# Kernel optimization log

Measured on AMD Instinct MI355X. Metric: run time of the kernel, lower is better.

The kernel has to match this reference:

```python
import jax, jax.numpy as jnp
import numpy as np

L, D_IN, D_MODEL, N_LAYERS = 4096, 8, 256, 2
ED, N, K = 512, 16, 4          # d_inner = 2*d_model, d_state, d_conv
DT_RANK = 16                   # ceil(d_model/16)
EPS = 1e-5


def setup_inputs() -> dict:
    key = jax.random.key(0)
    ks = jax.random.split(key, 10)
    def g(k, shape, s=0.02):
        return jax.random.normal(k, shape, jnp.float32) * s
    A_init = jnp.tile(jnp.arange(1, N + 1, dtype=jnp.float32), (N_LAYERS, ED, 1))
    return {
        "x": jax.random.normal(ks[0], (L, D_IN), jnp.float32),
        "fc_in_w": g(ks[1], (D_MODEL, D_IN), 0.1),
        "fc_in_b": jnp.zeros((D_MODEL,), jnp.float32),
        "fc_out_w": g(ks[2], (1, D_MODEL), 0.1),
        "fc_out_b": jnp.zeros((1,), jnp.float32),
        "norm_w": jnp.ones((N_LAYERS, D_MODEL), jnp.float32),
        "in_proj_w": g(ks[3], (N_LAYERS, 2 * ED, D_MODEL)),
        "conv_w": g(ks[4], (N_LAYERS, ED, 1, K), 0.1),
        "conv_b": jnp.zeros((N_LAYERS, ED), jnp.float32),
        "x_proj_w": g(ks[5], (N_LAYERS, DT_RANK + 2 * N, ED)),
        "dt_proj_w": g(ks[6], (N_LAYERS, ED, DT_RANK), 0.1),
        "dt_proj_b": jnp.full((N_LAYERS, ED), -4.0, jnp.float32),  # softplus(-4)~0.018
        "A_log": jnp.log(A_init),
        "D": jnp.ones((N_LAYERS, ED), jnp.float32),
        "out_proj_w": g(ks[7], (N_LAYERS, D_MODEL, ED)),
    }


def rmsnorm(x, w):
    return x * jax.lax.rsqrt(jnp.mean(x * x, axis=-1, keepdims=True) + EPS) * w


def causal_depthwise_conv(x, w, b):
    # x: [L, ED], w: [ED, 1, K] -> causal depthwise conv along L
    y = jax.lax.conv_general_dilated(
        x.T[None],  # [1, ED, L]
        w, (1,), [(K - 1, 0)],
        dimension_numbers=("NCH", "OIH", "NCH"),
        feature_group_count=ED)
    return y[0].T + b  # [L, ED]


def mamba_block(x, p):
    norm_w, in_w, cw, cb, xp_w, dtw, dtb, a_log, d, out_w = p
    xn = rmsnorm(x, norm_w)
    xz = xn @ in_w.T                      # [L, 2*ED]
    xi, z = xz[:, :ED], xz[:, ED:]
    xc = jax.nn.silu(causal_depthwise_conv(xi, cw, cb))   # [L, ED]
    dbc = xc @ xp_w.T                     # [L, DT_RANK + 2N]
    delta = jax.nn.softplus(dbc[:, :DT_RANK] @ dtw.T + dtb)  # [L, ED]
    B = dbc[:, DT_RANK:DT_RANK + N]       # [L, N]
    C = dbc[:, DT_RANK + N:]              # [L, N]
    A = -jnp.exp(a_log)                   # [ED, N]
    dA = jnp.exp(delta[:, :, None] * A[None])                 # [L, ED, N]
    dBx = delta[:, :, None] * B[:, None, :] * xc[:, :, None]  # [L, ED, N]

    def step(h, inp):
        da, dbx, c = inp
        h = da * h + dbx                  # [ED, N]
        return h, jnp.einsum("en,n->e", h, c)

    _, ys = jax.lax.scan(step, jnp.zeros((ED, N), x.dtype), (dA, dBx, C))
    y = (ys + d * xc) * jax.nn.silu(z)
    return x + y @ out_w.T


def forward(x, fc_in_w, fc_in_b, fc_out_w, fc_out_b, norm_w, in_proj_w, conv_w,
            conv_b, x_proj_w, dt_proj_w, dt_proj_b, A_log, D, out_proj_w):
    h = x @ fc_in_w.T + fc_in_b           # [L, D_MODEL]

    def layer(h, p):
        return mamba_block(h, p), None

    h, _ = jax.lax.scan(layer, h, (norm_w, in_proj_w, conv_w, conv_b, x_proj_w,
                                   dt_proj_w, dt_proj_b, A_log, D, out_proj_w))
    out = jnp.tanh(h @ fc_out_w.T + fc_out_b)  # [L, 1]
    return out.reshape(-1)


def reference(x, fc_in_w, fc_in_b, fc_out_w, fc_out_b, norm_w, in_proj_w, conv_w,
              conv_b, x_proj_w, dt_proj_w, dt_proj_b, A_log, D, out_proj_w):
    return forward(x, fc_in_w, fc_in_b, fc_out_w, fc_out_b, norm_w, in_proj_w,
                   conv_w, conv_b, x_proj_w, dt_proj_w, dt_proj_b, A_log, D,
                   out_proj_w)
```

## Files before the change

### kernel.cpp

```cpp
#include <hip/hip_runtime.h>
#include <math.h>

#define LSEQ 4096
#define D_IN 8
#define D_MODEL 256
#define ED 512
#define NSTATE 16
#define KCONV 4
#define DT_RANK 16
#define EPS 1e-5f
#define NCHUNK 256
#define CHUNK 16

typedef short short8 __attribute__((ext_vector_type(8)));
typedef unsigned short ushort8 __attribute__((ext_vector_type(8)));
typedef float f32x4 __attribute__((ext_vector_type(4)));

__device__ __forceinline__ float sigmoidf_(float x){ return 1.f/(1.f+__expf(-x)); }
__device__ __forceinline__ float siluf_(float x){ return x*sigmoidf_(x); }
__device__ __forceinline__ float softplusf_(float x){
  return (x > 20.f) ? x : log1pf(__expf(x));
}
__device__ __forceinline__ unsigned short f2bf(float f){
  unsigned int u = __float_as_uint(f);
  return (unsigned short)((u + 0x7fffu + ((u>>16)&1u)) >> 16);
}
__device__ __forceinline__ float bf2f(unsigned short u){
  return __uint_as_float(((unsigned int)u) << 16);
}

__global__ void k_prep(const float* __restrict__ x, const float* __restrict__ fiw,
                       const float* __restrict__ fib, const float* __restrict__ ipw,
                       const float* __restrict__ xpw, const float* __restrict__ opw,
                       float* __restrict__ h, unsigned short* __restrict__ wip,
                       unsigned short* __restrict__ wxp, unsigned short* __restrict__ wop){
  int b = blockIdx.x, tid = threadIdx.x;
  if (b < 2048) {
    int i = b*256 + tid;
    wip[i] = f2bf(ipw[i]);
    if (i < 2*48*ED)      wxp[i] = f2bf(xpw[i]);
    if (i < 2*D_MODEL*ED) wop[i] = f2bf(opw[i]);
  } else {
    int idx = (b-2048)*256 + tid;
    int t = idx >> 8, d = idx & 255;
    float acc = fib[d];
#pragma unroll
    for (int i = 0; i < D_IN; ++i) acc += x[t*D_IN+i]*fiw[d*D_IN+i];
    h[idx] = acc;
  }
}

template<int WM, int WN, bool RMS, bool ACC, bool ABF16, bool CBF16>
__global__ __launch_bounds__(256) void k_gemm_mfma(
    const void* __restrict__ Ap, const unsigned short* __restrict__ B,
    void* __restrict__ Cp, int M, int N, int K, const float* __restrict__ nwp)
{
  constexpr int BM = 32*WM, BN = 32*WN, LDT = 40;
  const float* A = (const float*)Ap;
  const unsigned short* Ab = (const unsigned short*)Ap;
  float* Cf = (float*)Cp;
  unsigned short* Cb = (unsigned short*)Cp;
  __shared__ unsigned short As[BM*LDT];
  __shared__ unsigned short Bs[BN*LDT];
  __shared__ float rms_lds[BM];
  __shared__ float nws[D_MODEL];
  const int tid = threadIdx.x;
  const int bm = blockIdx.x*BM, bn = blockIdx.y*BN;
  const int w = tid >> 6, lane = tid & 63;
  const int mb = (w>>1)*WM*16, nb = (w&1)*WN*16;
  const int lr = lane & 15, lk = (lane>>4)*8;
  if (RMS) {
    nws[tid] = nwp[tid];
    int row = tid >> 1, half = tid & 1;
    const float* ap = A + (size_t)(bm+row)*K + half*128;
    float s = 0.f;
#pragma unroll
    for (int i = 0; i < 128; i += 4) {
      float4 v = *(const float4*)&ap[i];
      s += v.x*v.x + v.y*v.y + v.z*v.z + v.w*v.w;
    }
    s += __shfl_xor(s, 1);
    if (!half) rms_lds[row] = rsqrtf(s*(1.f/D_MODEL) + EPS);
    __syncthreads();
  }
  f32x4 acc[WM][WN] = {};
  for (int k0 = 0; k0 < K; k0 += 32) {
#pragma unroll 2
    for (int s = tid; s < BM*4; s += 256) {
      int row = s>>2, kg = (s&3)*8;
      if (ABF16) {
        *(ushort8*)&As[row*LDT+kg] = *(const ushort8*)&Ab[(size_t)(bm+row)*K + k0 + kg];
      } else {
        const float* ap = &A[(size_t)(bm+row)*K + k0 + kg];
        float4 a0 = *(const float4*)ap, a1 = *(const float4*)(ap+4);
        if (RMS) {
          float rs = rms_lds[row];
          a0.x *= rs*nws[k0+kg+0]; a0.y *= rs*nws[k0+kg+1];
          a0.z *= rs*nws[k0+kg+2]; a0.w *= rs*nws[k0+kg+3];
          a1.x *= rs*nws[k0+kg+4]; a1.y *= rs*nws[k0+kg+5];
          a1.z *= rs*nws[k0+kg+6]; a1.w *= rs*nws[k0+kg+7];
        }
        ushort8 o;
        o[0]=f2bf(a0.x); o[1]=f2bf(a0.y); o[2]=f2bf(a0.z); o[3]=f2bf(a0.w);
        o[4]=f2bf(a1.x); o[5]=f2bf(a1.y); o[6]=f2bf(a1.z); o[7]=f2bf(a1.w);
        *(ushort8*)&As[row*LDT+kg] = o;
      }
    }
#pragma unroll 2
    for (int s = tid; s < BN*4; s += 256) {
      int row = s>>2, kg = (s&3)*8;
      ushort8 v = {0,0,0,0,0,0,0,0};
      if (bn+row < N) v = *(const ushort8*)&B[(size_t)(bn+row)*K + k0 + kg];
      *(ushort8*)&Bs[row*LDT+kg] = v;
    }
    __syncthreads();
    short8 af[WM], bfr[WN];
#pragma unroll
    for (int i = 0; i < WM; ++i) af[i]  = *(const short8*)&As[(mb+i*16+lr)*LDT + lk];
#pragma unroll
    for (int j = 0; j < WN; ++j) bfr[j] = *(const short8*)&Bs[(nb+j*16+lr)*LDT + lk];
#pragma unroll
    for (int i = 0; i < WM; ++i)
#pragma unroll
      for (int j = 0; j < WN; ++j)
        acc[i][j] = __builtin_amdgcn_mfma_f32_16x16x32_bf16(af[i], bfr[j], acc[i][j], 0, 0, 0);
    __syncthreads();
  }
#pragma unroll
  for (int i = 0; i < WM; ++i) {
#pragma unroll
    for (int j = 0; j < WN; ++j) {
      int col = bn + nb + j*16 + lr;
      if (col < N) {
#pragma unroll
        for (int r = 0; r < 4; ++r) {
          int row = bm + mb + i*16 + (lane>>4)*4 + r;
          size_t o = (size_t)row*N + col;
          if (CBF16)      Cb[o] = f2bf(acc[i][j][r]);
          else if (ACC)   Cf[o] = Cf[o] + acc[i][j][r];
          else            Cf[o] = acc[i][j][r];
        }
      }
    }
  }
}

__global__ __launch_bounds__(512) void k_cxps1(
    const unsigned short* __restrict__ xzb, const float* __restrict__ cw,
    const float* __restrict__ cb, const unsigned short* __restrict__ wxp,
    const float* __restrict__ dtw, const float* __restrict__ dtb,
    const float* __restrict__ alog, float* __restrict__ dbc,
    float* __restrict__ S, unsigned short* __restrict__ Q)
{
  constexpr int LDA = ED + 8;
  __shared__ unsigned short As[CHUNK*LDA];
  __shared__ float Ds[CHUNK][DT_RANK];
  __shared__ float Bsh[CHUNK][NSTATE];
  const int tid = threadIdx.x;
  const int e = tid;
  const int c = blockIdx.x;
  const int t0 = c*CHUNK;
  float cwv[KCONV];
#pragma unroll
  for (int k = 0; k < KCONV; ++k) cwv[k] = cw[e*KCONV+k];
  float cbv = cb[e];
  float w0=0.f, w1=0.f, w2=0.f;
  if (t0 > 0) {
    w0 = bf2f(xzb[(size_t)(t0-3)*(2*ED) + e]);
    w1 = bf2f(xzb[(size_t)(t0-2)*(2*ED) + e]);
    w2 = bf2f(xzb[(size_t)(t0-1)*(2*ED) + e]);
  }
  float xv[CHUNK];
#pragma unroll
  for (int t = 0; t < CHUNK; ++t) {
    float cur = bf2f(xzb[(size_t)(t0+t)*(2*ED) + e]);
    float v = siluf_(cbv + w0*cwv[0] + w1*cwv[1] + w2*cwv[2] + cur*cwv[3]);
    xv[t] = v;
    w0=w1; w1=w2; w2=cur;
  }
#pragma unroll
  for (int t = 0; t < CHUNK; ++t) {
    unsigned int us = f2bf(xv[t]);
    unsigned int other = (unsigned int)__shfl_down((int)us, 1);
    if ((tid & 1) == 0) *(unsigned int*)&As[t*LDA + e] = us | (other << 16);
  }
  __syncthreads();
  const int w = tid >> 6, lane = tid & 63;
  const int lr = lane & 15, lk = (lane>>4)*8;
  if (w < 3) {
    f32x4 acc = {};
#pragma unroll
    for (int ks = 0; ks < ED/32; ++ks) {
      short8 af = *(const short8*)&As[lr*LDA + ks*32 + lk];
      short8 bf = *(const short8*)&wxp[(size_t)(w*16+lr)*ED + ks*32 + lk];
      acc = __builtin_amdgcn_mfma_f32_16x16x32_bf16(af, bf, acc, 0, 0, 0);
    }
#pragma unroll
    for (int r = 0; r < 4; ++r) {
      int row = (lane>>4)*4 + r;
      dbc[(size_t)(t0+row)*48 + w*16 + lr] = acc[r];
      if (w == 0) Ds[row][lr] = acc[r];
      else if (w == 1) Bsh[row][lr] = acc[r];
    }
  }
  __syncthreads();
  float dtwv[DT_RANK];
#pragma unroll
  for (int r = 0; r < DT_RANK; ++r) dtwv[r] = dtw[e*DT_RANK+r];
  float dtbv = dtb[e];
  float A[NSTATE], h[NSTATE];
#pragma unroll
  for (int n = 0; n < NSTATE; ++n) { A[n] = -__expf(alog[e*NSTATE+n]); h[n] = 0.f; }
  float sd = 0.f;
#pragma unroll
  for (int t = 0; t < CHUNK; ++t) {
    float da = dtbv;
#pragma unroll
    for (int r = 0; r < DT_RANK; ++r) da += Ds[t][r]*dtwv[r];
    float d = softplusf_(da);
    sd += d;
    float dx = d*xv[t];
#pragma unroll
    for (int n = 0; n < NSTATE; ++n)
      h[n] = __expf(d*A[n])*h[n] + dx*Bsh[t][n];
  }
  S[(size_t)c*ED + e] = sd;
#pragma unroll
  for (int n = 0; n < NSTATE; ++n) Q[(size_t)(c*NSTATE+n)*ED + e] = f2bf(h[n]);
}

__global__ __launch_bounds__(256) void k_scan2(
    const float* __restrict__ alog, const float* __restrict__ S,
    unsigned short* __restrict__ Q)
{
  __shared__ float Pl[8][32], Rl[8][32], Hs[8][32];
  const int tid = threadIdx.x;
  const int seg = tid >> 5, chl = tid & 31;
  const int ch = blockIdx.x*32 + chl;
  const int n = ch >> 9, e = ch & 511;
  const float a = -__expf(alog[e*NSTATE+n]);
  const int c0 = seg*32;
  float ev[32], qv[32];
#pragma unroll
  for (int k = 0; k < 32; ++k) ev[k] = S[(size_t)(c0+k)*ED + e];
#pragma unroll
  for (int k = 0; k < 32; ++k) qv[k] = bf2f(Q[(size_t)((c0+k)*NSTATE+n)*ED + e]);
#pragma unroll
  for (int k = 0; k < 32; ++k) ev[k] = __expf(a*ev[k]);
  float P = 1.f, R = 0.f;
#pragma unroll
  for (int k = 0; k < 32; ++k) { R = ev[k]*R + qv[k]; P *= ev[k]; }
  Pl[seg][chl] = P; Rl[seg][chl] = R;
  __syncthreads();
  if (tid < 32) {
    float hcur = 0.f;
#pragma unroll
    for (int s = 0; s < 8; ++s) { Hs[s][tid] = hcur; hcur = Pl[s][tid]*hcur + Rl[s][tid]; }
  }
  __syncthreads();
  float h = Hs[seg][chl];
#pragma unroll
  for (int k = 0; k < 32; ++k) {
    float hl = qv[k];
    Q[(size_t)((c0+k)*NSTATE+n)*ED + e] = f2bf(h);
    h = ev[k]*h + hl;
  }
}

__global__ __launch_bounds__(512) void k_scan3(
    const unsigned short* __restrict__ xzb, const float* __restrict__ dbc,
    const float* __restrict__ cw, const float* __restrict__ cb,
    const float* __restrict__ dtw, const float* __restrict__ dtb,
    const float* __restrict__ alog, const unsigned short* __restrict__ Hin,
    const float* __restrict__ Dv, unsigned short* __restrict__ y)
{
  __shared__ float Ds[CHUNK][DT_RANK];
  __shared__ float Bsh[CHUNK][NSTATE];
  __shared__ float Cs[CHUNK][NSTATE];
  const int tid = threadIdx.x;
  const int e = tid;
  const int c = blockIdx.x;
  const int t0 = c*CHUNK;
  for (int i = tid; i < CHUNK*48; i += 512) {
    int t = i/48, col = i - t*48;
    float v = dbc[(size_t)(t0+t)*48 + col];
    if (col < DT_RANK) Ds[t][col] = v;
    else if (col < DT_RANK+NSTATE) Bsh[t][col-DT_RANK] = v;
    else Cs[t][col-DT_RANK-NSTATE] = v;
  }
  float cwv[KCONV];
#pragma unroll
  for (int k = 0; k < KCONV; ++k) cwv[k] = cw[e*KCONV+k];
  float cbv = cb[e];
  float w0=0.f, w1=0.f, w2=0.f;
  if (t0 > 0) {
    w0 = bf2f(xzb[(size_t)(t0-3)*(2*ED) + e]);
    w1 = bf2f(xzb[(size_t)(t0-2)*(2*ED) + e]);
    w2 = bf2f(xzb[(size_t)(t0-1)*(2*ED) + e]);
  }
  float x[CHUNK], z[CHUNK];
#pragma unroll
  for (int t = 0; t < CHUNK; ++t) {
    float cur = bf2f(xzb[(size_t)(t0+t)*(2*ED) + e]);
    x[t] = siluf_(cbv + w0*cwv[0] + w1*cwv[1] + w2*cwv[2] + cur*cwv[3]);
    w0=w1; w1=w2; w2=cur;
  }
#pragma unroll
  for (int t = 0; t < CHUNK; ++t) z[t] = bf2f(xzb[(size_t)(t0+t)*(2*ED) + ED + e]);
  __syncthreads();
  float dtwv[DT_RANK];
#pragma unroll
  for (int r = 0; r < DT_RANK; ++r) dtwv[r] = dtw[e*DT_RANK+r];
  float dtbv = dtb[e];
  float A[NSTATE], h[NSTATE];
#pragma unroll
  for (int n = 0; n < NSTATE; ++n) {
    A[n] = -__expf(alog[e*NSTATE+n]);
    h[n] = bf2f(Hin[(size_t)(c*NSTATE+n)*ED + e]);
  }
  float dv = Dv[e];
#pragma unroll
  for (int t = 0; t < CHUNK; ++t) {
    float da = dtbv;
#pragma unroll
    for (int r = 0; r < DT_RANK; ++r) da += Ds[t][r]*dtwv[r];
    float d = softplusf_(da);
    float dx = d*x[t];
    float ysum = 0.f;
#pragma unroll
    for (int n = 0; n < NSTATE; ++n) {
      h[n] = __expf(d*A[n])*h[n] + dx*Bsh[t][n];
      ysum += h[n]*Cs[t][n];
    }
    y[(size_t)(t0+t)*ED + e] = f2bf((ysum + dv*x[t]) * siluf_(z[t]));
  }
}

__global__ void k_fc_out(const float* __restrict__ h, const float* __restrict__ w,
                         const float* __restrict__ b, float* __restrict__ out){
  int wave = threadIdx.x >> 6, lane = threadIdx.x & 63;
  int row = blockIdx.x*4 + wave;
  const float4 hv = *(const float4*)&h[row*D_MODEL + lane*4];
  const float4 wv = *(const float4*)&w[lane*4];
  float s = hv.x*wv.x + hv.y*wv.y + hv.z*wv.z + hv.w*wv.w;
#pragma unroll
  for (int m = 32; m; m >>= 1) s += __shfl_xor(s, m);
  if (lane == 0) out[row] = tanhf(s + b[0]);
}

extern "C" void kernel_launch(void* const* d_in, const int* in_sizes, int n_in,
                              void* d_out, int out_size, void* d_ws, size_t ws_size,
                              hipStream_t stream){
  const float* x    = (const float*)d_in[0];
  const float* fiw  = (const float*)d_in[1];
  const float* fib  = (const float*)d_in[2];
  const float* fow  = (const float*)d_in[3];
  const float* fob  = (const float*)d_in[4];
  const float* nw   = (const float*)d_in[5];
  const float* ipw  = (const float*)d_in[6];
  const float* cw   = (const float*)d_in[7];
  const float* cb   = (const float*)d_in[8];
  const float* xpw  = (const float*)d_in[9];
  const float* dtw  = (const float*)d_in[10];
  const float* dtb  = (const float*)d_in[11];
  const float* alog = (const float*)d_in[12];
  const float* Dv   = (const float*)d_in[13];
  const float* opw  = (const float*)d_in[14];

  float* W = (float*)d_ws;
  float* h   = W;
  float* dbc = h   + (size_t)LSEQ*D_MODEL;
  float* S   = dbc + (size_t)LSEQ*48;
  unsigned short* xzb = (unsigned short*)(S + (size_t)NCHUNK*ED);
  unsigned short* Q   = xzb + (size_t)LSEQ*2*ED;
  unsigned short* yb  = Q   + (size_t)NCHUNK*NSTATE*ED;
  unsigned short* wip = yb  + (size_t)LSEQ*ED;
  unsigned short* wxp = wip + (size_t)2*2*ED*D_MODEL;
  unsigned short* wop = wxp + (size_t)2*48*ED;

  k_prep<<<2048 + LSEQ, 256, 0, stream>>>(x, fiw, fib, ipw, xpw, opw, h, wip, wxp, wop);

  for (int l = 0; l < 2; ++l) {
    const unsigned short* wip_l = wip + (size_t)l*2*ED*D_MODEL;
    const unsigned short* wxp_l = wxp + (size_t)l*48*ED;
    const unsigned short* wop_l = wop + (size_t)l*D_MODEL*ED;
    const float* nw_l   = nw   + l*D_MODEL;
    const float* cw_l   = cw   + l*ED*KCONV;
    const float* cb_l   = cb   + l*ED;
    const float* dtw_l  = dtw  + l*ED*DT_RANK;
    const float* dtb_l  = dtb  + l*ED;
    const float* alog_l = alog + l*ED*NSTATE;
    const float* D_l    = Dv   + l*ED;

    k_gemm_mfma<4,4,true,false,false,true><<<dim3(LSEQ/128, (2*ED)/128), 256, 0, stream>>>(
        h, wip_l, xzb, LSEQ, 2*ED, D_MODEL, nw_l);
    k_cxps1<<<NCHUNK, 512, 0, stream>>>(xzb, cw_l, cb_l, wxp_l, dtw_l, dtb_l, alog_l,
                                        dbc, S, Q);
    k_scan2<<<NCHUNK, 256, 0, stream>>>(alog_l, S, Q);
    k_scan3<<<NCHUNK, 512, 0, stream>>>(xzb, dbc, cw_l, cb_l, dtw_l, dtb_l, alog_l,
                                        Q, D_l, yb);
    k_gemm_mfma<2,2,false,true,true,false><<<dim3(LSEQ/64, D_MODEL/64), 256, 0, stream>>>(
        yb, wop_l, h, LSEQ, D_MODEL, ED, nullptr);
  }

  k_fc_out<<<LSEQ/4, 256, 0, stream>>>(h, fow, fob, (float*)d_out);
}
```

Before: 185.3 us.

## Fuse out_proj GEMM and fc_out head into the scan3 kernel

The selective-scan output kernel now keeps its 16x512 chunk of y in shared memory as bf16. It multiplies that chunk directly by the out_proj weights with MFMA and adds the result into the residual h. On the last layer it also computes the fc_out dot product and tanh in-kernel. This removes the global round-trip of y, one GEMM launch per layer and the final fc_out launch. In exchange, each block streams the full out_proj weight matrix from global/L2 without LDS tiling, and the GEMM work is spread over only 256 blocks.

```diff
diff --git a/kernel.cpp b/kernel.cpp
--- a/kernel.cpp
+++ b/kernel.cpp
@@ -50,16 +50,12 @@
   }
 }
 
-template<int WM, int WN, bool RMS, bool ACC, bool ABF16, bool CBF16>
-__global__ __launch_bounds__(256) void k_gemm_mfma(
-    const void* __restrict__ Ap, const unsigned short* __restrict__ B,
-    void* __restrict__ Cp, int M, int N, int K, const float* __restrict__ nwp)
+template<int WM, int WN>
+__global__ __launch_bounds__(256) void k_gemm_rms(
+    const float* __restrict__ A, const unsigned short* __restrict__ B,
+    unsigned short* __restrict__ Cb, int M, int N, int K, const float* __restrict__ nwp)
 {
   constexpr int BM = 32*WM, BN = 32*WN, LDT = 40;
-  const float* A = (const float*)Ap;
-  const unsigned short* Ab = (const unsigned short*)Ap;
-  float* Cf = (float*)Cp;
-  unsigned short* Cb = (unsigned short*)Cp;
   __shared__ unsigned short As[BM*LDT];
   __shared__ unsigned short Bs[BN*LDT];
   __shared__ float rms_lds[BM];
@@ -69,7 +65,7 @@
   const int w = tid >> 6, lane = tid & 63;
   const int mb = (w>>1)*WM*16, nb = (w&1)*WN*16;
   const int lr = lane & 15, lk = (lane>>4)*8;
-  if (RMS) {
+  {
     nws[tid] = nwp[tid];
     int row = tid >> 1, half = tid & 1;
     const float* ap = A + (size_t)(bm+row)*K + half*128;
@@ -88,30 +84,22 @@
 #pragma unroll 2
     for (int s = tid; s < BM*4; s += 256) {
       int row = s>>2, kg = (s&3)*8;
-      if (ABF16) {
-        *(ushort8*)&As[row*LDT+kg] = *(const ushort8*)&Ab[(size_t)(bm+row)*K + k0 + kg];
-      } else {
-        const float* ap = &A[(size_t)(bm+row)*K + k0 + kg];
-        float4 a0 = *(const float4*)ap, a1 = *(const float4*)(ap+4);
-        if (RMS) {
-          float rs = rms_lds[row];
-          a0.x *= rs*nws[k0+kg+0]; a0.y *= rs*nws[k0+kg+1];
-          a0.z *= rs*nws[k0+kg+2]; a0.w *= rs*nws[k0+kg+3];
-          a1.x *= rs*nws[k0+kg+4]; a1.y *= rs*nws[k0+kg+5];
-          a1.z *= rs*nws[k0+kg+6]; a1.w *= rs*nws[k0+kg+7];
-        }
-        ushort8 o;
-        o[0]=f2bf(a0.x); o[1]=f2bf(a0.y); o[2]=f2bf(a0.z); o[3]=f2bf(a0.w);
-        o[4]=f2bf(a1.x); o[5]=f2bf(a1.y); o[6]=f2bf(a1.z); o[7]=f2bf(a1.w);
-        *(ushort8*)&As[row*LDT+kg] = o;
-      }
+      const float* ap = &A[(size_t)(bm+row)*K + k0 + kg];
+      float4 a0 = *(const float4*)ap, a1 = *(const float4*)(ap+4);
+      float rs = rms_lds[row];
+      a0.x *= rs*nws[k0+kg+0]; a0.y *= rs*nws[k0+kg+1];
+      a0.z *= rs*nws[k0+kg+2]; a0.w *= rs*nws[k0+kg+3];
+      a1.x *= rs*nws[k0+kg+4]; a1.y *= rs*nws[k0+kg+5];
+      a1.z *= rs*nws[k0+kg+6]; a1.w *= rs*nws[k0+kg+7];
+      ushort8 o;
+      o[0]=f2bf(a0.x); o[1]=f2bf(a0.y); o[2]=f2bf(a0.z); o[3]=f2bf(a0.w);
+      o[4]=f2bf(a1.x); o[5]=f2bf(a1.y); o[6]=f2bf(a1.z); o[7]=f2bf(a1.w);
+      *(ushort8*)&As[row*LDT+kg] = o;
     }
 #pragma unroll 2
     for (int s = tid; s < BN*4; s += 256) {
       int row = s>>2, kg = (s&3)*8;
-      ushort8 v = {0,0,0,0,0,0,0,0};
-      if (bn+row < N) v = *(const ushort8*)&B[(size_t)(bn+row)*K + k0 + kg];
-      *(ushort8*)&Bs[row*LDT+kg] = v;
+      *(ushort8*)&Bs[row*LDT+kg] = *(const ushort8*)&B[(size_t)(bn+row)*K + k0 + kg];
     }
     __syncthreads();
     short8 af[WM], bfr[WN];
@@ -127,22 +115,16 @@
     __syncthreads();
   }
 #pragma unroll
-  for (int i = 0; i < WM; ++i) {
+  for (int i = 0; i < WM; ++i)
 #pragma unroll
     for (int j = 0; j < WN; ++j) {
       int col = bn + nb + j*16 + lr;
-      if (col < N) {
-#pragma unroll
-        for (int r = 0; r < 4; ++r) {
-          int row = bm + mb + i*16 + (lane>>4)*4 + r;
-          size_t o = (size_t)row*N + col;
-          if (CBF16)      Cb[o] = f2bf(acc[i][j][r]);
-          else if (ACC)   Cf[o] = Cf[o] + acc[i][j][r];
-          else            Cf[o] = acc[i][j][r];
-        }
+#pragma unroll
+      for (int r = 0; r < 4; ++r) {
+        int row = bm + mb + i*16 + (lane>>4)*4 + r;
+        Cb[(size_t)row*N + col] = f2bf(acc[i][j][r]);
       }
     }
-  }
 }
 
 __global__ __launch_bounds__(512) void k_cxps1(
@@ -267,16 +249,23 @@
   }
 }
 
-__global__ __launch_bounds__(512) void k_scan3(
+template<bool FC>
+__global__ __launch_bounds__(512) void k_scan3op(
     const unsigned short* __restrict__ xzb, const float* __restrict__ dbc,
     const float* __restrict__ cw, const float* __restrict__ cb,
     const float* __restrict__ dtw, const float* __restrict__ dtb,
     const float* __restrict__ alog, const unsigned short* __restrict__ Hin,
-    const float* __restrict__ Dv, unsigned short* __restrict__ y)
+    const float* __restrict__ Dv, const unsigned short* __restrict__ wop,
+    float* __restrict__ h, const float* __restrict__ fow,
+    const float* __restrict__ fob, float* __restrict__ out)
 {
+  constexpr int LDY = ED + 8;
+  constexpr int LDH = D_MODEL + 4;
+  __shared__ unsigned short Ys[CHUNK*LDY];
   __shared__ float Ds[CHUNK][DT_RANK];
   __shared__ float Bsh[CHUNK][NSTATE];
   __shared__ float Cs[CHUNK][NSTATE];
+  __shared__ float Hsh[CHUNK*LDH];
   const int tid = threadIdx.x;
   const int e = tid;
   const int c = blockIdx.x;
@@ -312,13 +301,14 @@
 #pragma unroll
   for (int r = 0; r < DT_RANK; ++r) dtwv[r] = dtw[e*DT_RANK+r];
   float dtbv = dtb[e];
-  float A[NSTATE], h[NSTATE];
+  float A[NSTATE], hs[NSTATE];
 #pragma unroll
   for (int n = 0; n < NSTATE; ++n) {
     A[n] = -__expf(alog[e*NSTATE+n]);
-    h[n] = bf2f(Hin[(size_t)(c*NSTATE+n)*ED + e]);
+    hs[n] = bf2f(Hin[(size_t)(c*NSTATE+n)*ED + e]);
   }
   float dv = Dv[e];
+  float yv[CHUNK];
 #pragma unroll
   for (int t = 0; t < CHUNK; ++t) {
     float da = dtbv;
@@ -329,23 +319,56 @@
     float ysum = 0.f;
 #pragma unroll
     for (int n = 0; n < NSTATE; ++n) {
-      h[n] = __expf(d*A[n])*h[n] + dx*Bsh[t][n];
-      ysum += h[n]*Cs[t][n];
-    }
-    y[(size_t)(t0+t)*ED + e] = f2bf((ysum + dv*x[t]) * siluf_(z[t]));
-  }
-}
-
-__global__ void k_fc_out(const float* __restrict__ h, const float* __restrict__ w,
-                         const float* __restrict__ b, float* __restrict__ out){
-  int wave = threadIdx.x >> 6, lane = threadIdx.x & 63;
-  int row = blockIdx.x*4 + wave;
-  const float4 hv = *(const float4*)&h[row*D_MODEL + lane*4];
-  const float4 wv = *(const float4*)&w[lane*4];
-  float s = hv.x*wv.x + hv.y*wv.y + hv.z*wv.z + hv.w*wv.w;
-#pragma unroll
-  for (int m = 32; m; m >>= 1) s += __shfl_xor(s, m);
-  if (lane == 0) out[row] = tanhf(s + b[0]);
+      hs[n] = __expf(d*A[n])*hs[n] + dx*Bsh[t][n];
+      ysum += hs[n]*Cs[t][n];
+    }
+    yv[t] = (ysum + dv*x[t]) * siluf_(z[t]);
+  }
+#pragma unroll
+  for (int t = 0; t < CHUNK; ++t) {
+    unsigned int us = f2bf(yv[t]);
+    unsigned int other = (unsigned int)__shfl_down((int)us, 1);
+    if ((tid & 1) == 0) *(unsigned int*)&Ys[t*LDY + e] = us | (other << 16);
+  }
+  __syncthreads();
+  const int w = tid >> 6, lane = tid & 63;
+  const int lr = lane & 15, lk = (lane>>4)*8;
+  f32x4 acc[2] = {};
+#pragma unroll
+  for (int j = 0; j < 2; ++j) {
+    int ct = w*2 + j;
+#pragma unroll
+    for (int ks = 0; ks < ED/32; ++ks) {
+      short8 af = *(const short8*)&Ys[lr*LDY + ks*32 + lk];
+      short8 bf = *(const short8*)&wop[(size_t)(ct*16+lr)*ED + ks*32 + lk];
+      acc[j] = __builtin_amdgcn_mfma_f32_16x16x32_bf16(af, bf, acc[j], 0, 0, 0);
+    }
+  }
+#pragma unroll
+  for (int j = 0; j < 2; ++j) {
+    int col = w*32 + j*16 + lr;
+#pragma unroll
+    for (int r = 0; r < 4; ++r) {
+      int row = (lane>>4)*4 + r;
+      size_t o = (size_t)(t0+row)*D_MODEL + col;
+      float v = h[o] + acc[j][r];
+      if (FC) Hsh[row*LDH + col] = v;
+      else    h[o] = v;
+    }
+  }
+  if (FC) {
+    __syncthreads();
+    int row = tid >> 5, l5 = tid & 31;
+    float s = 0.f;
+#pragma unroll
+    for (int i = 0; i < 8; ++i) {
+      int col = l5*8 + i;
+      s += Hsh[row*LDH + col]*fow[col];
+    }
+#pragma unroll
+    for (int m = 16; m; m >>= 1) s += __shfl_xor(s, m);
+    if (l5 == 0) out[t0+row] = tanhf(s + fob[0]);
+  }
 }
 
 extern "C" void kernel_launch(void* const* d_in, const int* in_sizes, int n_in,
@@ -373,8 +396,7 @@
   float* S   = dbc + (size_t)LSEQ*48;
   unsigned short* xzb = (unsigned short*)(S + (size_t)NCHUNK*ED);
   unsigned short* Q   = xzb + (size_t)LSEQ*2*ED;
-  unsigned short* yb  = Q   + (size_t)NCHUNK*NSTATE*ED;
-  unsigned short* wip = yb  + (size_t)LSEQ*ED;
+  unsigned short* wip = Q   + (size_t)NCHUNK*NSTATE*ED;
   unsigned short* wxp = wip + (size_t)2*2*ED*D_MODEL;
   unsigned short* wop = wxp + (size_t)2*48*ED;
 
@@ -392,16 +414,16 @@
     const float* alog_l = alog + l*ED*NSTATE;
     const float* D_l    = Dv   + l*ED;
 
-    k_gemm_mfma<4,4,true,false,false,true><<<dim3(LSEQ/128, (2*ED)/128), 256, 0, stream>>>(
+    k_gemm_rms<4,4><<<dim3(LSEQ/128, (2*ED)/128), 256, 0, stream>>>(
         h, wip_l, xzb, LSEQ, 2*ED, D_MODEL, nw_l);
     k_cxps1<<<NCHUNK, 512, 0, stream>>>(xzb, cw_l, cb_l, wxp_l, dtw_l, dtb_l, alog_l,
                                         dbc, S, Q);
     k_scan2<<<NCHUNK, 256, 0, stream>>>(alog_l, S, Q);
-    k_scan3<<<NCHUNK, 512, 0, stream>>>(xzb, dbc, cw_l, cb_l, dtw_l, dtb_l, alog_l,
-                                        Q, D_l, yb);
-    k_gemm_mfma<2,2,false,true,true,false><<<dim3(LSEQ/64, D_MODEL/64), 256, 0, stream>>>(
-        yb, wop_l, h, LSEQ, D_MODEL, ED, nullptr);
-  }
-
-  k_fc_out<<<LSEQ/4, 256, 0, stream>>>(h, fow, fob, (float*)d_out);
-}
+    if (l == 0)
+      k_scan3op<false><<<NCHUNK, 512, 0, stream>>>(xzb, dbc, cw_l, cb_l, dtw_l, dtb_l,
+          alog_l, Q, D_l, wop_l, h, fow, fob, (float*)d_out);
+    else
+      k_scan3op<true><<<NCHUNK, 512, 0, stream>>>(xzb, dbc, cw_l, cb_l, dtw_l, dtb_l,
+          alog_l, Q, D_l, wop_l, h, fow, fob, (float*)d_out);
+  }
+}
```

Measured after the change: 255.5 us. 37.9% more time.
